# Performance work log

Hardware: AMD Instinct MI355X
Metric: run time of the kernel (lower is better)

## Reference

```python
import jax, jax.numpy as jnp
import numpy as np
import math

B, T, C, H = 4, 2048, 1024, 16

def setup_inputs() -> dict:
    key = jax.random.key(0)
    k1, k2, k3 = jax.random.split(key, 3)
    scale = 1.0 / math.sqrt(C)
    return {
        "x": jax.random.normal(k1, (B, T, C), dtype=jnp.float32),
        "w_attn": jax.random.normal(k2, (C, 3 * C), dtype=jnp.float32) * scale,
        "b_attn": jnp.zeros((3 * C,), dtype=jnp.float32),
        "w_proj": jax.random.normal(k3, (C, C), dtype=jnp.float32) * scale,
        "b_proj": jnp.zeros((C,), dtype=jnp.float32),
    }

def reference(x, w_attn, b_attn, w_proj, b_proj):
    Bq, Tq, Cq = x.shape
    hd = Cq // H  # head dim
    qkv = x @ w_attn + b_attn                       # [B,T,3C]
    q, k, v = jnp.split(qkv, 3, axis=-1)
    # [B,T,C] -> [B,H,T,hd]
    q = q.reshape(Bq, Tq, H, hd).transpose(0, 2, 1, 3)
    k = k.reshape(Bq, Tq, H, hd).transpose(0, 2, 1, 3)
    v = v.reshape(Bq, Tq, H, hd).transpose(0, 2, 1, 3)
    att = jnp.einsum('bhqd,bhkd->bhqk', q, k) * (1.0 / math.sqrt(hd))
    causal = jnp.tril(jnp.ones((Tq, Tq), dtype=bool))
    att = jnp.where(causal[None, None], att, -jnp.inf)
    att = jax.nn.softmax(att, axis=-1)              # dropout p=0 (eval)
    y = jnp.einsum('bhqk,bhkd->bhqd', att, v)       # [B,H,T,hd]
    y = y.transpose(0, 2, 1, 3).reshape(Bq, Tq, Cq)
    return y @ w_proj + b_proj
```

## Files before the change

### kernel.cpp

```cpp
#include <hip/hip_runtime.h>


#define T_SEQ 2048
#define NB 4
#define NH 16
#define CDIM 1024
#define HD 64
#define BH (NB * NH)
#define QSCALE 0.1803368801111204f

typedef float f32x4 __attribute__((ext_vector_type(4)));
typedef float f32x16 __attribute__((ext_vector_type(16)));
typedef __bf16 bf16x8 __attribute__((ext_vector_type(8)));
typedef unsigned short u16x8 __attribute__((ext_vector_type(8)));
typedef unsigned short u16x4 __attribute__((ext_vector_type(4)));

__device__ __forceinline__ unsigned short f2b(float f) {
    union { float f; unsigned u; } v; v.f = f;
    unsigned u = v.u;
    u += 0x7FFFu + ((u >> 16) & 1u);
    return (unsigned short)(u >> 16);
}

__device__ __forceinline__ f32x4 fzero4() {
    f32x4 z; z[0] = 0.f; z[1] = 0.f; z[2] = 0.f; z[3] = 0.f; return z;
}

__device__ __forceinline__ f32x16 mfma32(bf16x8 a, bf16x8 b, f32x16 c) {
    return __builtin_amdgcn_mfma_f32_32x32x16_bf16(a, b, c, 0, 0, 0);
}

__device__ __forceinline__ void gld16(const void* gp, void* lp) {
    __builtin_amdgcn_global_load_lds(
        (const __attribute__((address_space(1))) unsigned int*)gp,
        (__attribute__((address_space(3))) unsigned int*)lp, 16, 0, 0);
}

__global__ __launch_bounds__(256) void cast_f32_bf16_kernel(
        const float* __restrict__ in, unsigned short* __restrict__ out, int n8) {
    int i = blockIdx.x * 256 + threadIdx.x;
    int stride = gridDim.x * 256;
    for (; i < n8; i += stride) {
        const float4* p = reinterpret_cast<const float4*>(in) + (size_t)i * 2;
        float4 a = p[0], b = p[1];
        u16x8 o;
        o[0] = f2b(a.x); o[1] = f2b(a.y); o[2] = f2b(a.z); o[3] = f2b(a.w);
        o[4] = f2b(b.x); o[5] = f2b(b.y); o[6] = f2b(b.z); o[7] = f2b(b.w);
        *(reinterpret_cast<u16x8*>(out) + i) = o;
    }
}

__global__ __launch_bounds__(256) void transpose_cast_kernel(
        const float* __restrict__ in, unsigned short* __restrict__ out, int R, int C) {
    __shared__ unsigned short tile[32][33];
    int tx = threadIdx.x, ty = threadIdx.y;
    int c0 = blockIdx.x * 32, r0 = blockIdx.y * 32;
    for (int rr = ty; rr < 32; rr += 8)
        tile[rr][tx] = f2b(in[(size_t)(r0 + rr) * C + c0 + tx]);
    __syncthreads();
    for (int rr = ty; rr < 32; rr += 8)
        out[(size_t)(c0 + rr) * R + r0 + tx] = tile[tx][rr];
}

template <int EPI>
__global__ __launch_bounds__(256) void gemm_bt_kernel(
        const unsigned short* __restrict__ A, const unsigned short* __restrict__ Bt,
        const float* __restrict__ bias, float* __restrict__ outF,
        unsigned short* __restrict__ q_out, unsigned short* __restrict__ k_out,
        unsigned short* __restrict__ v_out, int M, int N, int K) {
    __shared__ alignas(16) unsigned short As[2][128 * 32];
    __shared__ alignas(16) unsigned short Bs[2][128 * 32];

    int tid = threadIdx.x;
    int wid = tid >> 6, lane = tid & 63;
    int g = lane >> 4, lc = lane & 15;
    int wr = (wid >> 1) * 64, wc = (wid & 1) * 64;
    int m0 = blockIdx.y * 128, n0 = blockIdx.x * 128;

    f32x4 acc[4][4];
#pragma unroll
    for (int m = 0; m < 4; ++m)
#pragma unroll
        for (int n = 0; n < 4; ++n) acc[m][n] = fzero4();

    int srow = tid >> 2;
    int scol = (tid & 3) * 8;
    const unsigned short* Ap = A + (size_t)(m0 + srow) * K + scol;
    const unsigned short* Bp = Bt + (size_t)(n0 + srow) * K + scol;
    int ldst = (wid * 16) * 32;
    int ldst2 = (64 + wid * 16) * 32;

#define GSTAGE(BUF, KOFF)                                      \
    gld16(Ap + (KOFF), &As[BUF][ldst]);                        \
    gld16(Ap + (size_t)64 * K + (KOFF), &As[BUF][ldst2]);      \
    gld16(Bp + (KOFF), &Bs[BUF][ldst]);                        \
    gld16(Bp + (size_t)64 * K + (KOFF), &Bs[BUF][ldst2]);

    GSTAGE(0, 0)
    __syncthreads();

    int nk = K >> 5;
    for (int it = 0; it < nk; ++it) {
        int cur = it & 1;
        if (it + 1 < nk) { GSTAGE(cur ^ 1, (it + 1) << 5) }

        bf16x8 af[4], bfr[4];
#pragma unroll
        for (int m = 0; m < 4; ++m)
            af[m] = *(const bf16x8*)&As[cur][(wr + m * 16 + lc) * 32 + g * 8];
#pragma unroll
        for (int n = 0; n < 4; ++n)
            bfr[n] = *(const bf16x8*)&Bs[cur][(wc + n * 16 + lc) * 32 + g * 8];
#pragma unroll
        for (int m = 0; m < 4; ++m)
#pragma unroll
            for (int n = 0; n < 4; ++n)
                acc[m][n] = __builtin_amdgcn_mfma_f32_16x16x32_bf16(af[m], bfr[n], acc[m][n], 0, 0, 0);

        __syncthreads();
    }
#undef GSTAGE

#pragma unroll
    for (int m = 0; m < 4; ++m) {
        int rowb = m0 + wr + m * 16 + g * 4;
#pragma unroll
        for (int n = 0; n < 4; ++n) {
            int col = n0 + wc + n * 16 + lc;
            float bv = bias[col];
            if (EPI == 0) {
#pragma unroll
                for (int i = 0; i < 4; ++i)
                    outF[(size_t)(rowb + i) * N + col] = acc[m][n][i] + bv;
            } else {
                int which = col >> 10;
                int c = col & 1023;
                int h = c >> 6, d = c & 63;
                int bh_ = (rowb >> 11) * NH + h;
                int tl = rowb & 2047;
                if (which == 2) {
                    u16x4 vq;
#pragma unroll
                    for (int i = 0; i < 4; ++i) vq[i] = f2b(acc[m][n][i] + bv);
                    *(u16x4*)&v_out[(size_t)bh_ * (HD * T_SEQ) + (size_t)d * T_SEQ + tl] = vq;
                } else {
                    unsigned short* dst = which ? k_out : q_out;
                    float sc = which ? 1.0f : QSCALE;
#pragma unroll
                    for (int i = 0; i < 4; ++i)
                        dst[((size_t)bh_ * T_SEQ + tl + i) * HD + d] =
                            f2b((acc[m][n][i] + bv) * sc);
                }
            }
        }
    }
}

__global__ __launch_bounds__(256, 4) void attn32_kernel(
        const unsigned short* __restrict__ Qb, const unsigned short* __restrict__ Kb,
        const unsigned short* __restrict__ Vt, unsigned short* __restrict__ Yb) {
    __shared__ alignas(16) char smem[32768];

    int tid = threadIdx.x;
    int wid = tid >> 6, lane = tid & 63;
    int ql = lane & 31, hi = lane >> 5;
    int ql7 = ql & 7;

    int id = blockIdx.x;
    int x = id & 7;
    int k = id >> 3;
    int r = k >> 5;
    int c = k & 31;
    int hh = 2 * r + (c >> 4);
    int j = c & 15;
    int qg = (r & 1) ? (15 - j) : j;
    int bh = x * 8 + hh;
    size_t hb = (size_t)bh * (T_SEQ * HD);

    int qt = qg * 4 + wid;
    int q0 = qt * 32;
    int ktMax = qt >> 1;
    int ntB = 2 * qg + 2;

    bf16x8 qf[4];
    const unsigned short* Qp = Qb + hb + (size_t)(q0 + ql) * HD + hi * 8;
#pragma unroll
    for (int d = 0; d < 4; ++d) qf[d] = *(const bf16x8*)(Qp + d * 16);

    f32x16 zz;
#pragma unroll
    for (int rr = 0; rr < 16; ++rr) zz[rr] = 0.f;
    f32x16 o0 = zz, o1 = zz;
    float mi = -__builtin_inff(), li = 0.f;

    int r8 = lane >> 3;
    int sslot8 = ((lane & 7) ^ r8) * 8;
    const unsigned short* Kg = Kb + hb + (size_t)(wid * 16 + r8) * HD + sslot8;
    const unsigned short* Vg = Vt + hb + (size_t)(wid * 16 + r8) * T_SEQ + sslot8;

    gld16(Kg, smem + wid * 2048);
    gld16(Kg + 8 * HD, smem + wid * 2048 + 1024);
    gld16(Vg, smem + 8192 + wid * 2048);
    gld16(Vg + 8 * T_SEQ, smem + 8192 + wid * 2048 + 1024);
    __syncthreads();

#define KF(K0, D) (*(const bf16x8*)&KB_[(((K0)*32 + ql) << 6) + ((((D)*2 + hi) ^ ql7) << 3)])
#define VF(DB, T) (*(const bf16x8*)&VB_[(((DB)*32 + ql) << 6) + ((((T)*2 + hi) ^ ql7) << 3)])

    for (int kt = 0; kt < ntB; ++kt) {
        int cur = kt & 1;
        if (kt + 1 < ntB) {
            char* nb = smem + (cur ^ 1) * 16384;
            gld16(Kg + (size_t)(kt + 1) * 64 * HD, nb + wid * 2048);
            gld16(Kg + (size_t)((kt + 1) * 64 + 8) * HD, nb + wid * 2048 + 1024);
            gld16(Vg + (kt + 1) * 64, nb + 8192 + wid * 2048);
            gld16(Vg + (kt + 1) * 64 + 8 * T_SEQ, nb + 8192 + wid * 2048 + 1024);
        }
        if (kt <= ktMax) {
            const unsigned short* KB_ = (const unsigned short*)(smem + cur * 16384);
            const unsigned short* VB_ = (const unsigned short*)(smem + cur * 16384 + 8192);
            int k0 = kt * 64;

            f32x16 s0_, s1_;
            __builtin_amdgcn_s_setprio(1);
            s0_ = mfma32(KF(0, 0), qf[0], zz);
            s0_ = mfma32(KF(0, 1), qf[1], s0_);
            s0_ = mfma32(KF(0, 2), qf[2], s0_);
            s0_ = mfma32(KF(0, 3), qf[3], s0_);
            s1_ = mfma32(KF(1, 0), qf[0], zz);
            s1_ = mfma32(KF(1, 1), qf[1], s1_);
            s1_ = mfma32(KF(1, 2), qf[2], s1_);
            s1_ = mfma32(KF(1, 3), qf[3], s1_);
            __builtin_amdgcn_s_setprio(0);

            if (kt == ktMax) {
                int qg_ = q0 + ql;
#pragma unroll
                for (int rr = 0; rr < 16; ++rr) {
                    int kof_ = k0 + 8 * (rr >> 2) + (rr & 3) + 4 * hi;
                    if (kof_ > qg_) s0_[rr] = -__builtin_inff();
                    if (kof_ + 32 > qg_) s1_[rr] = -__builtin_inff();
                }
            }

            float t_[8];
#pragma unroll
            for (int rr = 0; rr < 8; ++rr)
                t_[rr] = fmaxf(fmaxf(s0_[rr], s0_[rr + 8]), fmaxf(s1_[rr], s1_[rr + 8]));
#pragma unroll
            for (int rr = 0; rr < 4; ++rr) t_[rr] = fmaxf(t_[rr], t_[rr + 4]);
            float pm_ = fmaxf(fmaxf(t_[0], t_[1]), fmaxf(t_[2], t_[3]));
            pm_ = fmaxf(pm_, __shfl_xor(pm_, 32));

            float mn_ = mi;
            if (!__all((int)(pm_ <= mi + 8.f))) {
                mn_ = fmaxf(mi, pm_);
                float f_ = __builtin_amdgcn_exp2f(mi - mn_);
                mi = mn_;
                li *= f_;
                o0 *= f_;
                o1 *= f_;
            }
#pragma unroll
            for (int rr = 0; rr < 16; ++rr) {
                s0_[rr] = __builtin_amdgcn_exp2f(s0_[rr] - mn_);
                s1_[rr] = __builtin_amdgcn_exp2f(s1_[rr] - mn_);
            }
            float u_[8];
#pragma unroll
            for (int rr = 0; rr < 8; ++rr)
                u_[rr] = (s0_[rr] + s0_[rr + 8]) + (s1_[rr] + s1_[rr + 8]);
#pragma unroll
            for (int rr = 0; rr < 4; ++rr) u_[rr] += u_[rr + 4];
            float ps_ = (u_[0] + u_[1]) + (u_[2] + u_[3]);
            ps_ += __shfl_xor(ps_, 32);
            li += ps_;

#pragma unroll
            for (int K0_ = 0; K0_ < 2; ++K0_) {
#pragma unroll
                for (int h2_ = 0; h2_ < 2; ++h2_) {
                    float e0_ = K0_ ? s1_[8 * h2_ + 0] : s0_[8 * h2_ + 0];
                    float e1_ = K0_ ? s1_[8 * h2_ + 1] : s0_[8 * h2_ + 1];
                    float e2_ = K0_ ? s1_[8 * h2_ + 2] : s0_[8 * h2_ + 2];
                    float e3_ = K0_ ? s1_[8 * h2_ + 3] : s0_[8 * h2_ + 3];
                    float e4_ = K0_ ? s1_[8 * h2_ + 4] : s0_[8 * h2_ + 4];
                    float e5_ = K0_ ? s1_[8 * h2_ + 5] : s0_[8 * h2_ + 5];
                    float e6_ = K0_ ? s1_[8 * h2_ + 6] : s0_[8 * h2_ + 6];
                    float e7_ = K0_ ? s1_[8 * h2_ + 7] : s0_[8 * h2_ + 7];
                    unsigned a_, b_, c_, d_;
                    asm("v_cvt_pk_bf16_f32 %0, %1, %2" : "=v"(a_) : "v"(e0_), "v"(e1_));
                    asm("v_cvt_pk_bf16_f32 %0, %1, %2" : "=v"(b_) : "v"(e2_), "v"(e3_));
                    asm("v_cvt_pk_bf16_f32 %0, %1, %2" : "=v"(c_) : "v"(e4_), "v"(e5_));
                    asm("v_cvt_pk_bf16_f32 %0, %1, %2" : "=v"(d_) : "v"(e6_), "v"(e7_));
                    asm("v_permlane32_swap_b32 %0, %1" : "+v"(a_), "+v"(c_));
                    asm("v_permlane32_swap_b32 %0, %1" : "+v"(b_), "+v"(d_));
                    union { unsigned u[4]; bf16x8 v; } pf_;
                    pf_.u[0] = a_; pf_.u[1] = b_; pf_.u[2] = c_; pf_.u[3] = d_;
                    __builtin_amdgcn_s_setprio(1);
                    o0 = mfma32(VF(0, K0_ * 2 + h2_), pf_.v, o0);
                    o1 = mfma32(VF(1, K0_ * 2 + h2_), pf_.v, o1);
                    __builtin_amdgcn_s_setprio(0);
                }
            }
        }
        __syncthreads();
    }
#undef KF
#undef VF

    int bb = bh >> 4, h = bh & 15;
    float iv = 1.0f / li;
#pragma unroll
    for (int dblk = 0; dblk < 2; ++dblk) {
#pragma unroll
        for (int a = 0; a < 4; ++a) {
            u16x4 wv;
#pragma unroll
            for (int i = 0; i < 4; ++i)
                wv[i] = f2b((dblk ? o1[4 * a + i] : o0[4 * a + i]) * iv);
            int dq = dblk * 32 + 8 * a + 4 * hi;
            *(u16x4*)&Yb[((size_t)(bb * T_SEQ + q0 + ql)) * CDIM + h * HD + dq] = wv;
        }
    }
}

extern "C" void kernel_launch(void* const* d_in, const int* in_sizes, int n_in,
                              void* d_out, int out_size, void* d_ws, size_t ws_size,
                              hipStream_t stream) {
    const float* x      = (const float*)d_in[0];
    const float* w_attn = (const float*)d_in[1];
    const float* b_attn = (const float*)d_in[2];
    const float* w_proj = (const float*)d_in[3];
    const float* b_proj = (const float*)d_in[4];
    float* out = (float*)d_out;

    char* ws = (char*)d_ws;
    unsigned short* xb  = (unsigned short*)(ws);
    unsigned short* wTa = (unsigned short*)(ws + 16777216);
    unsigned short* wTp = (unsigned short*)(ws + 23068672);
    unsigned short* qb  = (unsigned short*)(ws + 25165824);
    unsigned short* kb  = (unsigned short*)(ws + 41943040);
    unsigned short* vTb = (unsigned short*)(ws + 58720256);
    unsigned short* yb  = xb;

    cast_f32_bf16_kernel<<<2048, 256, 0, stream>>>(x, xb, (NB * T_SEQ * CDIM) / 8);
    transpose_cast_kernel<<<dim3(3072 / 32, 1024 / 32), dim3(32, 8), 0, stream>>>(
        w_attn, wTa, 1024, 3072);
    transpose_cast_kernel<<<dim3(1024 / 32, 1024 / 32), dim3(32, 8), 0, stream>>>(
        w_proj, wTp, 1024, 1024);

    gemm_bt_kernel<1><<<dim3(3072 / 128, 8192 / 128), 256, 0, stream>>>(
        xb, wTa, b_attn, nullptr, qb, kb, vTb, 8192, 3072, 1024);

    attn32_kernel<<<dim3(1024), 256, 0, stream>>>(qb, kb, vTb, yb);

    gemm_bt_kernel<0><<<dim3(1024 / 128, 8192 / 128), 256, 0, stream>>>(
        yb, wTp, b_proj, out, nullptr, nullptr, nullptr, 8192, 1024, 1024);
}
```

Before: 174.0 us.

## Replace 128x128 GEMM with 256x256 tiled, swizzled, pipelined 8-wave kernel

Rewrites both projection GEMMs to use 256x256 block tiles with 512 threads, a 64-wide K step, an XOR-swizzled LDS layout and double-buffered global-to-LDS loads. The loads are interleaved with MFMA quadrants using explicit waitcnt, barrier and setprio scheduling, and block IDs are remapped across 8 groups to improve L2 locality. This aims to raise operand reuse and overlap memory with compute, at the cost of 128KB of LDS, fewer blocks (128 for the output projection, fewer than CUs) and fragile hand-written synchronisation.

```diff
diff --git a/kernel.cpp b/kernel.cpp
--- a/kernel.cpp
+++ b/kernel.cpp
@@ -35,6 +35,11 @@
         (const __attribute__((address_space(1))) unsigned int*)gp,
         (__attribute__((address_space(3))) unsigned int*)lp, 16, 0, 0);
 }
+
+#define VMCNT2 do { asm volatile("s_waitcnt vmcnt(2)" ::: "memory"); __builtin_amdgcn_sched_barrier(0); } while (0)
+#define VMCNT0 do { asm volatile("s_waitcnt vmcnt(0)" ::: "memory"); __builtin_amdgcn_sched_barrier(0); } while (0)
+#define LGKM0  do { asm volatile("s_waitcnt lgkmcnt(0)" ::: "memory"); __builtin_amdgcn_sched_barrier(0); } while (0)
+#define BARRIER do { asm volatile("" ::: "memory"); __builtin_amdgcn_s_barrier(); __builtin_amdgcn_sched_barrier(0); } while (0)
 
 __global__ __launch_bounds__(256) void cast_f32_bf16_kernel(
         const float* __restrict__ in, unsigned short* __restrict__ out, int n8) {
@@ -63,75 +68,130 @@
 }
 
 template <int EPI>
-__global__ __launch_bounds__(256) void gemm_bt_kernel(
+__global__ __launch_bounds__(512, 2) void gemm256_kernel(
         const unsigned short* __restrict__ A, const unsigned short* __restrict__ Bt,
         const float* __restrict__ bias, float* __restrict__ outF,
         unsigned short* __restrict__ q_out, unsigned short* __restrict__ k_out,
-        unsigned short* __restrict__ v_out, int M, int N, int K) {
-    __shared__ alignas(16) unsigned short As[2][128 * 32];
-    __shared__ alignas(16) unsigned short Bs[2][128 * 32];
+        unsigned short* __restrict__ v_out, int M, int N, int K, int nbx) {
+    __shared__ alignas(16) char smem[131072];
 
     int tid = threadIdx.x;
     int wid = tid >> 6, lane = tid & 63;
-    int g = lane >> 4, lc = lane & 15;
-    int wr = (wid >> 1) * 64, wc = (wid & 1) * 64;
-    int m0 = blockIdx.y * 128, n0 = blockIdx.x * 128;
-
-    f32x4 acc[4][4];
-#pragma unroll
-    for (int m = 0; m < 4; ++m)
-#pragma unroll
-        for (int n = 0; n < 4; ++n) acc[m][n] = fzero4();
-
-    int srow = tid >> 2;
-    int scol = (tid & 3) * 8;
-    const unsigned short* Ap = A + (size_t)(m0 + srow) * K + scol;
-    const unsigned short* Bp = Bt + (size_t)(n0 + srow) * K + scol;
-    int ldst = (wid * 16) * 32;
-    int ldst2 = (64 + wid * 16) * 32;
-
-#define GSTAGE(BUF, KOFF)                                      \
-    gld16(Ap + (KOFF), &As[BUF][ldst]);                        \
-    gld16(Ap + (size_t)64 * K + (KOFF), &As[BUF][ldst2]);      \
-    gld16(Bp + (KOFF), &Bs[BUF][ldst]);                        \
-    gld16(Bp + (size_t)64 * K + (KOFF), &Bs[BUF][ldst2]);
-
-    GSTAGE(0, 0)
-    __syncthreads();
-
-    int nk = K >> 5;
-    for (int it = 0; it < nk; ++it) {
-        int cur = it & 1;
-        if (it + 1 < nk) { GSTAGE(cur ^ 1, (it + 1) << 5) }
-
-        bf16x8 af[4], bfr[4];
-#pragma unroll
-        for (int m = 0; m < 4; ++m)
-            af[m] = *(const bf16x8*)&As[cur][(wr + m * 16 + lc) * 32 + g * 8];
-#pragma unroll
-        for (int n = 0; n < 4; ++n)
-            bfr[n] = *(const bf16x8*)&Bs[cur][(wc + n * 16 + lc) * 32 + g * 8];
-#pragma unroll
-        for (int m = 0; m < 4; ++m)
-#pragma unroll
-            for (int n = 0; n < 4; ++n)
-                acc[m][n] = __builtin_amdgcn_mfma_f32_16x16x32_bf16(af[m], bfr[n], acc[m][n], 0, 0, 0);
-
-        __syncthreads();
+    int wm = wid >> 2, wn = wid & 3;
+    int lc = lane & 15, g = lane >> 4;
+    int g16 = g << 4;
+    int bchunk = 2 + (wn >> 1);
+    int bofs = (wn & 1) * 64;
+
+    int id = blockIdx.x;
+    int cpx = gridDim.x >> 3;
+    int swz = (id & 7) * cpx + (id >> 3);
+    int by = swz / nbx, bx = swz - by * nbx;
+    int m0 = by * 256, n0 = bx * 256;
+
+    f32x4 acc[8][4];
+#pragma unroll
+    for (int i = 0; i < 8; ++i)
+#pragma unroll
+        for (int j = 0; j < 4; ++j) acc[i][j] = fzero4();
+
+    int r8 = lane >> 3;
+    int scol = ((lane & 7) ^ r8) * 8;
+    const unsigned short* Agl = A + (size_t)(m0 + r8) * K + scol;
+    const unsigned short* Bgl = Bt + (size_t)(n0 + r8) * K + scol;
+
+#define STAGE(SLOT, C, KT) do {                                                     \
+        const unsigned short* gp_ = ((C) < 2 ? Agl : Bgl)                           \
+            + (size_t)(((C) & 1) * 128) * K + (size_t)(KT) * 64;                    \
+        char* lb_ = smem + ((((SLOT) * 4) + (C)) << 14) + (wid << 10);              \
+        gld16(gp_ + (size_t)(wid * 8) * K, lb_);                                    \
+        gld16(gp_ + (size_t)(64 + wid * 8) * K, lb_ + 8192);                        \
+    } while (0)
+
+    struct QSub { bf16x8 a[4][2]; bf16x8 b[2][2]; };
+    QSub sub0, sub1;
+
+#define LOADQ(DST, SLOT, QM, QN) do {                                               \
+        const char* Ab_ = smem + ((((SLOT) * 4) + wm) << 14);                       \
+        _Pragma("unroll")                                                           \
+        for (int i_ = 0; i_ < 4; ++i_) {                                            \
+            int row_ = ((QM) * 4 + i_) * 16 + lc;                                   \
+            int rb_ = row_ << 7, r7_ = (row_ & 7) << 4;                             \
+            DST.a[i_][0] = *(const bf16x8*)(Ab_ + rb_ + (g16 ^ r7_));               \
+            DST.a[i_][1] = *(const bf16x8*)(Ab_ + rb_ + ((64 + g16) ^ r7_));        \
+        }                                                                           \
+        const char* Bb_ = smem + ((((SLOT) * 4) + bchunk) << 14);                   \
+        _Pragma("unroll")                                                           \
+        for (int i_ = 0; i_ < 2; ++i_) {                                            \
+            int row_ = bofs + ((QN) * 2 + i_) * 16 + lc;                            \
+            int rb_ = row_ << 7, r7_ = (row_ & 7) << 4;                             \
+            DST.b[i_][0] = *(const bf16x8*)(Bb_ + rb_ + (g16 ^ r7_));               \
+            DST.b[i_][1] = *(const bf16x8*)(Bb_ + rb_ + ((64 + g16) ^ r7_));        \
+        }                                                                           \
+    } while (0)
+
+#define DOQ(SRC, QM, QN) do {                                                       \
+        __builtin_amdgcn_s_setprio(1);                                              \
+        _Pragma("unroll")                                                           \
+        for (int i_ = 0; i_ < 4; ++i_)                                              \
+            _Pragma("unroll")                                                       \
+            for (int j_ = 0; j_ < 2; ++j_) {                                        \
+                acc[(QM) * 4 + i_][(QN) * 2 + j_] =                                 \
+                    __builtin_amdgcn_mfma_f32_16x16x32_bf16(                        \
+                        SRC.a[i_][0], SRC.b[j_][0],                                 \
+                        acc[(QM) * 4 + i_][(QN) * 2 + j_], 0, 0, 0);                \
+                acc[(QM) * 4 + i_][(QN) * 2 + j_] =                                 \
+                    __builtin_amdgcn_mfma_f32_16x16x32_bf16(                        \
+                        SRC.a[i_][1], SRC.b[j_][1],                                 \
+                        acc[(QM) * 4 + i_][(QN) * 2 + j_], 0, 0, 0);                \
+            }                                                                       \
+        __builtin_amdgcn_s_setprio(0);                                              \
+    } while (0)
+
+    int nt = K >> 6;
+
+    STAGE(0, 0, 0); STAGE(0, 1, 0); STAGE(0, 2, 0); STAGE(0, 3, 0);
+    STAGE(1, 0, 1);
+    VMCNT2;
+    BARRIER;
+    LOADQ(sub0, 0, 0, 0);
+
+    for (int t = 0; t < nt; ++t) {
+        int sl = t & 1, sl2 = sl ^ 1;
+        bool more1 = (t + 1 < nt), more2 = (t + 2 < nt);
+        LOADQ(sub1, sl, 0, 1);
+        if (more1) STAGE(sl2, 1, t + 1);
+        DOQ(sub0, 0, 0);
+        LGKM0; BARRIER;
+        LOADQ(sub0, sl, 1, 0);
+        if (more1) STAGE(sl2, 2, t + 1);
+        DOQ(sub1, 0, 1);
+        LGKM0; BARRIER;
+        LOADQ(sub1, sl, 1, 1);
+        if (more1) STAGE(sl2, 3, t + 1);
+        DOQ(sub0, 1, 0);
+        LGKM0; BARRIER;
+        if (more2) { STAGE(sl, 0, t + 2); VMCNT2; } else { VMCNT0; }
+        BARRIER;
+        if (more1) LOADQ(sub0, sl2, 0, 0);
+        DOQ(sub1, 1, 1);
+        LGKM0; BARRIER;
     }
-#undef GSTAGE
-
-#pragma unroll
-    for (int m = 0; m < 4; ++m) {
-        int rowb = m0 + wr + m * 16 + g * 4;
-#pragma unroll
-        for (int n = 0; n < 4; ++n) {
-            int col = n0 + wc + n * 16 + lc;
+#undef STAGE
+#undef LOADQ
+#undef DOQ
+
+#pragma unroll
+    for (int fm = 0; fm < 8; ++fm) {
+        int rowb = m0 + wm * 128 + fm * 16 + g * 4;
+#pragma unroll
+        for (int fn = 0; fn < 4; ++fn) {
+            int col = n0 + wn * 64 + fn * 16 + lc;
             float bv = bias[col];
             if (EPI == 0) {
 #pragma unroll
                 for (int i = 0; i < 4; ++i)
-                    outF[(size_t)(rowb + i) * N + col] = acc[m][n][i] + bv;
+                    outF[(size_t)(rowb + i) * N + col] = acc[fm][fn][i] + bv;
             } else {
                 int which = col >> 10;
                 int c = col & 1023;
@@ -141,7 +201,7 @@
                 if (which == 2) {
                     u16x4 vq;
 #pragma unroll
-                    for (int i = 0; i < 4; ++i) vq[i] = f2b(acc[m][n][i] + bv);
+                    for (int i = 0; i < 4; ++i) vq[i] = f2b(acc[fm][fn][i] + bv);
                     *(u16x4*)&v_out[(size_t)bh_ * (HD * T_SEQ) + (size_t)d * T_SEQ + tl] = vq;
                 } else {
                     unsigned short* dst = which ? k_out : q_out;
@@ -149,7 +209,7 @@
 #pragma unroll
                     for (int i = 0; i < 4; ++i)
                         dst[((size_t)bh_ * T_SEQ + tl + i) * HD + d] =
-                            f2b((acc[m][n][i] + bv) * sc);
+                            f2b((acc[fm][fn][i] + bv) * sc);
                 }
             }
         }
@@ -350,11 +410,11 @@
     transpose_cast_kernel<<<dim3(1024 / 32, 1024 / 32), dim3(32, 8), 0, stream>>>(
         w_proj, wTp, 1024, 1024);
 
-    gemm_bt_kernel<1><<<dim3(3072 / 128, 8192 / 128), 256, 0, stream>>>(
-        xb, wTa, b_attn, nullptr, qb, kb, vTb, 8192, 3072, 1024);
+    gemm256_kernel<1><<<dim3(384), 512, 0, stream>>>(
+        xb, wTa, b_attn, nullptr, qb, kb, vTb, 8192, 3072, 1024, 12);
 
     attn32_kernel<<<dim3(1024), 256, 0, stream>>>(qb, kb, vTb, yb);
 
-    gemm_bt_kernel<0><<<dim3(1024 / 128, 8192 / 128), 256, 0, stream>>>(
-        yb, wTp, b_proj, out, nullptr, nullptr, nullptr, 8192, 1024, 1024);
-}
+    gemm256_kernel<0><<<dim3(128), 512, 0, stream>>>(
+        yb, wTp, b_proj, out, nullptr, nullptr, nullptr, 8192, 1024, 1024, 4);
+}
```

After: 198.4 us. +14.0%, slower.

## Add 256x256-tile QKV GEMM with swizzled LDS, block remap and interleaved prefetch

Applied to the files above, without the earlier changes.

Replaces the 128x128 QKV projection GEMM with a new 512-thread kernel that computes 256x256 output tiles. It uses an XOR-swizzled LDS layout to reduce bank conflicts, remaps block IDs for L2 locality, and splits the next-tile global-to-LDS loads between two halves of the MFMA work, with s_setprio around the MFMA bursts. The larger tile improves operand reuse per LDS load, but it raises register pressure and leaves only 384 blocks. The output projection keeps the old kernel with its template removed.

```diff
diff --git a/kernel.cpp b/kernel.cpp
--- a/kernel.cpp
+++ b/kernel.cpp
@@ -24,6 +24,10 @@
 
 __device__ __forceinline__ f32x4 fzero4() {
     f32x4 z; z[0] = 0.f; z[1] = 0.f; z[2] = 0.f; z[3] = 0.f; return z;
+}
+
+__device__ __forceinline__ f32x4 mfma16(bf16x8 a, bf16x8 b, f32x4 c) {
+    return __builtin_amdgcn_mfma_f32_16x16x32_bf16(a, b, c, 0, 0, 0);
 }
 
 __device__ __forceinline__ f32x16 mfma32(bf16x8 a, bf16x8 b, f32x16 c) {
@@ -62,12 +66,124 @@
         out[(size_t)(c0 + rr) * R + r0 + tx] = tile[tx][rr];
 }
 
-template <int EPI>
+__global__ __launch_bounds__(512, 2) void gemm256_kernel(
+        const unsigned short* __restrict__ A, const unsigned short* __restrict__ Bt,
+        const float* __restrict__ bias,
+        unsigned short* __restrict__ q_out, unsigned short* __restrict__ k_out,
+        unsigned short* __restrict__ v_out, int M, int N, int K, int nbx) {
+    __shared__ alignas(16) char smem[65536];
+
+    int tid = threadIdx.x;
+    int wid = tid >> 6, lane = tid & 63;
+    int wm = wid >> 2, wn = wid & 3;
+    int lc = lane & 15, g = lane >> 4;
+    int gp = g ^ ((lc >> 1) & 3);
+
+    int id = blockIdx.x;
+    int cpx = gridDim.x >> 3;
+    int swz = (id & 7) * cpx + (id >> 3);
+    int by = swz / nbx, bx = swz - by * nbx;
+    int m0 = by * 256, n0 = bx * 256;
+
+    f32x4 acc[8][4];
+#pragma unroll
+    for (int i = 0; i < 8; ++i)
+#pragma unroll
+        for (int j = 0; j < 4; ++j) acc[i][j] = fzero4();
+
+    int srow = tid >> 2;
+    int scol = ((tid & 3) ^ ((srow >> 1) & 3)) * 8;
+    const unsigned short* Agl = A + (size_t)(m0 + srow) * K + scol;
+    const unsigned short* Bgl = Bt + (size_t)(n0 + srow) * K + scol;
+
+#define STAGE_A(SLOT, KT) do {                                   \
+        const unsigned short* g_ = Agl + (size_t)(KT) * 32;      \
+        char* l_ = smem + (SLOT) * 32768 + wid * 1024;           \
+        gld16(g_, l_);                                           \
+        gld16(g_ + (size_t)128 * K, l_ + 8192);                  \
+    } while (0)
+#define STAGE_B(SLOT, KT) do {                                   \
+        const unsigned short* g_ = Bgl + (size_t)(KT) * 32;      \
+        char* l_ = smem + (SLOT) * 32768 + 16384 + wid * 1024;   \
+        gld16(g_, l_);                                           \
+        gld16(g_ + (size_t)128 * K, l_ + 8192);                  \
+    } while (0)
+
+    int aoff = (wm * 128 + lc) * 64 + gp * 16;
+    int boff = 16384 + (wn * 64 + lc) * 64 + gp * 16;
+
+    STAGE_A(0, 0); STAGE_B(0, 0);
+    __syncthreads();
+
+    int nt = K >> 5;
+    for (int t = 0; t < nt; ++t) {
+        const char* sb = smem + (t & 1) * 32768;
+        bool more = (t + 1 < nt);
+        int sl2 = (t & 1) ^ 1;
+
+        bf16x8 a0[4], b0[4];
+#pragma unroll
+        for (int i = 0; i < 4; ++i) a0[i] = *(const bf16x8*)(sb + aoff + i * 1024);
+#pragma unroll
+        for (int j = 0; j < 4; ++j) b0[j] = *(const bf16x8*)(sb + boff + j * 1024);
+        if (more) STAGE_A(sl2, t + 1);
+        __builtin_amdgcn_s_setprio(1);
+#pragma unroll
+        for (int i = 0; i < 4; ++i)
+#pragma unroll
+            for (int j = 0; j < 4; ++j)
+                acc[i][j] = mfma16(a0[i], b0[j], acc[i][j]);
+        __builtin_amdgcn_s_setprio(0);
+
+        bf16x8 a1[4];
+#pragma unroll
+        for (int i = 0; i < 4; ++i) a1[i] = *(const bf16x8*)(sb + aoff + (4 + i) * 1024);
+        if (more) STAGE_B(sl2, t + 1);
+        __builtin_amdgcn_s_setprio(1);
+#pragma unroll
+        for (int i = 0; i < 4; ++i)
+#pragma unroll
+            for (int j = 0; j < 4; ++j)
+                acc[4 + i][j] = mfma16(a1[i], b0[j], acc[4 + i][j]);
+        __builtin_amdgcn_s_setprio(0);
+
+        __syncthreads();
+    }
+#undef STAGE_A
+#undef STAGE_B
+
+#pragma unroll
+    for (int fm = 0; fm < 8; ++fm) {
+        int rowb = m0 + wm * 128 + fm * 16 + g * 4;
+#pragma unroll
+        for (int fn = 0; fn < 4; ++fn) {
+            int col = n0 + wn * 64 + fn * 16 + lc;
+            float bv = bias[col];
+            int which = col >> 10;
+            int c = col & 1023;
+            int h = c >> 6, d = c & 63;
+            int bh_ = (rowb >> 11) * NH + h;
+            int tl = rowb & 2047;
+            if (which == 2) {
+                u16x4 vq;
+#pragma unroll
+                for (int i = 0; i < 4; ++i) vq[i] = f2b(acc[fm][fn][i] + bv);
+                *(u16x4*)&v_out[(size_t)bh_ * (HD * T_SEQ) + (size_t)d * T_SEQ + tl] = vq;
+            } else {
+                unsigned short* dst = which ? k_out : q_out;
+                float sc = which ? 1.0f : QSCALE;
+#pragma unroll
+                for (int i = 0; i < 4; ++i)
+                    dst[((size_t)bh_ * T_SEQ + tl + i) * HD + d] =
+                        f2b((acc[fm][fn][i] + bv) * sc);
+            }
+        }
+    }
+}
+
 __global__ __launch_bounds__(256) void gemm_bt_kernel(
         const unsigned short* __restrict__ A, const unsigned short* __restrict__ Bt,
-        const float* __restrict__ bias, float* __restrict__ outF,
-        unsigned short* __restrict__ q_out, unsigned short* __restrict__ k_out,
-        unsigned short* __restrict__ v_out, int M, int N, int K) {
+        const float* __restrict__ bias, float* __restrict__ outF, int M, int N, int K) {
     __shared__ alignas(16) unsigned short As[2][128 * 32];
     __shared__ alignas(16) unsigned short Bs[2][128 * 32];
 
@@ -83,10 +199,8 @@
 #pragma unroll
         for (int n = 0; n < 4; ++n) acc[m][n] = fzero4();
 
-    int srow = tid >> 2;
-    int scol = (tid & 3) * 8;
-    const unsigned short* Ap = A + (size_t)(m0 + srow) * K + scol;
-    const unsigned short* Bp = Bt + (size_t)(n0 + srow) * K + scol;
+    const unsigned short* Ap = A + (size_t)(m0 + (tid >> 2)) * K + (tid & 3) * 8;
+    const unsigned short* Bp = Bt + (size_t)(n0 + (tid >> 2)) * K + (tid & 3) * 8;
     int ldst = (wid * 16) * 32;
     int ldst2 = (64 + wid * 16) * 32;
 
@@ -115,7 +229,7 @@
         for (int m = 0; m < 4; ++m)
 #pragma unroll
             for (int n = 0; n < 4; ++n)
-                acc[m][n] = __builtin_amdgcn_mfma_f32_16x16x32_bf16(af[m], bfr[n], acc[m][n], 0, 0, 0);
+                acc[m][n] = mfma16(af[m], bfr[n], acc[m][n]);
 
         __syncthreads();
     }
@@ -128,30 +242,9 @@
         for (int n = 0; n < 4; ++n) {
             int col = n0 + wc + n * 16 + lc;
             float bv = bias[col];
-            if (EPI == 0) {
-#pragma unroll
-                for (int i = 0; i < 4; ++i)
-                    outF[(size_t)(rowb + i) * N + col] = acc[m][n][i] + bv;
-            } else {
-                int which = col >> 10;
-                int c = col & 1023;
-                int h = c >> 6, d = c & 63;
-                int bh_ = (rowb >> 11) * NH + h;
-                int tl = rowb & 2047;
-                if (which == 2) {
-                    u16x4 vq;
-#pragma unroll
-                    for (int i = 0; i < 4; ++i) vq[i] = f2b(acc[m][n][i] + bv);
-                    *(u16x4*)&v_out[(size_t)bh_ * (HD * T_SEQ) + (size_t)d * T_SEQ + tl] = vq;
-                } else {
-                    unsigned short* dst = which ? k_out : q_out;
-                    float sc = which ? 1.0f : QSCALE;
-#pragma unroll
-                    for (int i = 0; i < 4; ++i)
-                        dst[((size_t)bh_ * T_SEQ + tl + i) * HD + d] =
-                            f2b((acc[m][n][i] + bv) * sc);
-                }
-            }
+#pragma unroll
+            for (int i = 0; i < 4; ++i)
+                outF[(size_t)(rowb + i) * N + col] = acc[m][n][i] + bv;
         }
     }
 }
@@ -350,11 +443,11 @@
     transpose_cast_kernel<<<dim3(1024 / 32, 1024 / 32), dim3(32, 8), 0, stream>>>(
         w_proj, wTp, 1024, 1024);
 
-    gemm_bt_kernel<1><<<dim3(3072 / 128, 8192 / 128), 256, 0, stream>>>(
-        xb, wTa, b_attn, nullptr, qb, kb, vTb, 8192, 3072, 1024);
+    gemm256_kernel<<<dim3(384), 512, 0, stream>>>(
+        xb, wTa, b_attn, qb, kb, vTb, 8192, 3072, 1024, 12);
 
     attn32_kernel<<<dim3(1024), 256, 0, stream>>>(qb, kb, vTb, yb);
 
-    gemm_bt_kernel<0><<<dim3(1024 / 128, 8192 / 128), 256, 0, stream>>>(
-        yb, wTp, b_proj, out, nullptr, nullptr, nullptr, 8192, 1024, 1024);
-}
+    gemm_bt_kernel<<<dim3(1024 / 128, 8192 / 128), 256, 0, stream>>>(
+        yb, wTp, b_proj, out, 8192, 1024, 1024);
+}
```

Result: no change. 176.9 us (+1.7%).
